# Performance work log

Hardware: AMD Instinct MI355X
Metric: run time of the kernel (lower is better)

Reference implementation:

```python
import math
from functools import partial

import jax
import jax.numpy as jnp
import numpy as np

DS = 128            # domain_size (cells per side); original used 600
PD = 1.0            # particle diameter d == grid spacing
KN = 500000.0       # normal stiffness
MASS = 1.0
DT = 1e-4
FS = 5              # filter (stencil) size -> 5x5x5 shifts
_ALPHA = -math.log(0.7) / math.pi
_GAMMA = _ALPHA / math.sqrt(_ALPHA ** 2 + 1.0)
ETA = 2.0 * _GAMMA * math.sqrt(KN * MASS)   # damping_coefficient_Eta
EPS = 1e-4          # torch.clamp(dist, 0.0001)
SHAPE = (1, 1, DS, DS, DS)


def setup_inputs() -> dict:
    rng = np.random.default_rng(0)
    occ = np.zeros((DS, DS, DS), np.float32)
    occ[1:-1, 1:-1, 1:-1] = (rng.random((DS - 2,) * 3) < 0.2).astype(np.float32)
    iz, iy, ix = np.meshgrid(np.arange(DS), np.arange(DS), np.arange(DS), indexing="ij")
    jit = lambda: (rng.random((DS,) * 3).astype(np.float32) - 0.5) * 0.4
    # occupied cells store their own coordinate (+jitter) so round(x/d) == cell index
    x = (occ * (ix.astype(np.float32) + jit())).astype(np.float32)
    y = (occ * (iy.astype(np.float32) + jit())).astype(np.float32)
    z = (occ * (iz.astype(np.float32) + jit())).astype(np.float32)
    vel = lambda: (occ * rng.normal(0.0, 0.5, (DS,) * 3)).astype(np.float32)
    asg = lambda a: jnp.asarray(a.reshape(SHAPE))
    return {
        "x_grid": asg(x), "y_grid": asg(y), "z_grid": asg(z),
        "vx_grid": asg(vel()), "vy_grid": asg(vel()), "vz_grid": asg(vel()),
        "mask": asg(occ),
    }


def _contrib(xg, yg, zg, vxg, vyg, vzg, shift):
    """Force contribution from one (i,j,k) stencil shift (torch.roll based)."""
    roll = lambda g: jnp.roll(g, shift, axis=(2, 3, 4))
    dx, dy, dz = xg - roll(xg), yg - roll(yg), zg - roll(zg)
    sq = dx * dx + dy * dy + dz * dz
    dist = jnp.sqrt(sq + 1e-20)  # tiny eps keeps sqrt grad finite at sq==0; value unchanged in fp32
    cd = jnp.maximum(dist, EPS)  # torch.clamp(dist, 0.0001)
    vn = ((vxg - roll(vxg)) * dx + (vyg - roll(vyg)) * dy + (vzg - roll(vzg)) * dz) / cd
    ov = dist < 2.0 * PD
    fx = jnp.where(ov, KN * (dist - 2.0 * PD) * dx / cd + ETA * vn * dx / cd, 0.0)
    fy = jnp.where(ov, KN * (dist - 2.0 * PD) * dy / cd + ETA * vn * dy / cd, 0.0)
    fz = jnp.where(ov, KN * (dist - 2.0 * PD) * dz / cd + ETA * vn * dz / cd, 0.0)
    return fx, fy, fz


def _forward(xg, yg, zg, vxg, vyg, vzg, mask):
    f32 = jnp.float32
    fx = jnp.zeros(SHAPE, f32)
    fy = jnp.zeros(SHAPE, f32)
    fz = jnp.zeros(SHAPE, f32)
    for i in range(FS):
        for j in range(FS):
            for k in range(FS):
                c = jax.checkpoint(partial(_contrib, shift=(k - 2, j - 2, i - 2)))
                dfx, dfy, dfz = c(xg, yg, zg, vxg, vyg, vzg)
                fx, fy, fz = fx + dfx, fy + dfy, fz + dfz
    # boundary overlap forces
    bl = ((xg != 0.0) & (xg < PD)).astype(f32)
    br = (xg > DS - 2.0 * PD).astype(f32)
    bb = ((yg != 0.0) & (yg < PD)).astype(f32)
    bt = (yg > DS - 2.0 * PD).astype(f32)
    bf = ((zg != 0.0) & (zg < PD)).astype(f32)
    bk = (zg > DS - 2.0 * PD).astype(f32)
    fxb = KN * bl * mask * (PD - xg) - KN * br * mask * (xg - DS + 2.0 * PD) - ETA * vxg * bl * mask - ETA * vxg * br * mask
    fyb = KN * bb * mask * (PD - yg) - KN * bt * mask * (yg - DS + 2.0 * PD) - ETA * vyg * bb * mask - ETA * vyg * bt * mask
    fzb = KN * bf * mask * (PD - zg) - KN * bk * mask * (zg - DS + 2.0 * PD) - ETA * vzg * bf * mask - ETA * vzg * bk * mask
    vxn = vxg + DT / MASS * mask * (-0.0 * MASS - fx + fxb)
    vyn = vyg + DT / MASS * mask * (-9.8 * MASS - fy + fyb)
    vzn = vzg + DT / MASS * mask * (-0.0 * MASS - fz + fzb)
    cell = lambda g: jnp.round(g / PD).astype(jnp.int32)
    cx0, cy0, cz0 = cell(xg), cell(yg), cell(zg)
    xn, yn, zn = xg + DT * vxn, yg + DT * vyn, zg + DT * vzn
    cx1, cy1, cz1 = cell(xn), cell(yn), cell(zn)
    # cell-list relocation: flatten to linear indices; invalid (empty) cells -> dump slot D3
    D3 = DS ** 3
    def lin(cz, cy, cx):
        v = (cx != 0) & (cy != 0) & (cz != 0)   # torch filters cell_* != 0
        return jnp.where(v, (cz * DS + cy) * DS + cx, D3).reshape(-1)
    lo = lin(cz0, cy0, cx0)
    ln = lin(cz1, cy1, cx1)
    pad = lambda g: jnp.concatenate([g.reshape(-1), jnp.zeros((1,), g.dtype)])
    unpad = lambda f: f[:D3].reshape(SHAPE)
    def move(g):
        gf = pad(g)
        return unpad(gf.at[lo].set(0.0).at[ln].set(gf[lo]))
    mask_n = unpad(pad(mask).at[lo].set(0.0).at[ln].set(1.0))
    return (move(xn), move(yn), move(zn), move(vxn), move(vyn), move(vzn), mask_n)


def reference(x_grid, y_grid, z_grid, vx_grid, vy_grid, vz_grid, mask):
    return _forward(x_grid, y_grid, z_grid, vx_grid, vy_grid, vz_grid, mask)
```

## Files before the change

kernel.cpp:

```cpp
#include <hip/hip_runtime.h>

#define DSZ   128
#define DMSK  127
#define D3    (DSZ * DSZ * DSZ)

#define KN_F   500000.0f
#define ETA_F  159.535258f
#define DT_F   1e-4f

#define TBX   32
#define TBY   4
#define TBZ   4
#define HALO  2
#define RS    37
#define PS    296
#define SLOTS 2368
#define NT    512
#define NHALO (36 * 8 * 8)
#define RES_S 520

struct OffTabs { int a[36]; int b[48]; int e[44]; };
constexpr OffTabs make_tabs() {
    OffTabs t{}; int na = 0, nb = 0, ne = 0;
    for (int dz = -2; dz <= 2; ++dz)
        for (int dy = -2; dy <= 2; ++dy)
            for (int dx = -2; dx <= 2; ++dx) {
                const int r2 = dz*dz + dy*dy + dx*dx;
                const int off = dz * PS + dy * RS + dx;
                if (r2 <= 4)      t.a[na++] = off;
                else if (r2 <= 6) t.b[nb++] = off;
                else              t.e[ne++] = off;
            }
    while (na < 36) t.a[na++] = 0;
    return t;
}
__constant__ OffTabs g_tabs = make_tabs();

__device__ __forceinline__ unsigned bf16_rne(float f) {
    unsigned u = __float_as_uint(f);
    u += 0x7fffu + ((u >> 16) & 1u);
    return u >> 16;
}
__device__ __forceinline__ unsigned packvv(float vy, float vz) {
    return bf16_rne(vy) | (bf16_rne(vz) << 16);
}
__device__ __forceinline__ float unpk_lo(unsigned w) { return __uint_as_float(w << 16); }
__device__ __forceinline__ float unpk_hi(unsigned w) { return __uint_as_float(w & 0xffff0000u); }

__device__ __forceinline__ void pair_full(
    const float4* __restrict__ lsp, const unsigned* __restrict__ lsv, int n,
    float px, float py, float pz, float vx, float vy, float vz,
    float& fx, float& fy, float& fz)
{
    const float4 q = lsp[n];
    const float ddx = px - q.x, ddy = py - q.y, ddz = pz - q.z;
    const float sq  = fmaf(ddx, ddx, fmaf(ddy, ddy, fmaf(ddz, ddz, 1e-20f)));
    const float rsd = __builtin_amdgcn_rsqf(sq);
    const float dist = sq * rsd;
    const unsigned w = lsv[n];
    const float vn = (fmaf(vx - q.w, ddx, fmaf(vy - unpk_lo(w), ddy, (vz - unpk_hi(w)) * ddz))) * rsd;
    float coef = fmaf(KN_F, dist - 2.0f, ETA_F * vn) * rsd;
    coef = (sq < 4.0f) ? coef : 0.0f;
    fx = fmaf(coef, ddx, fx);
    fy = fmaf(coef, ddy, fy);
    fz = fmaf(coef, ddz, fz);
}

__global__ __launch_bounds__(NT) void dem_tile(
    const float* __restrict__ X, const float* __restrict__ Y, const float* __restrict__ Z,
    const float* __restrict__ VX, const float* __restrict__ VY, const float* __restrict__ VZ,
    float* __restrict__ out)
{
    __shared__ float4 lsp[SLOTS];
    __shared__ unsigned lsv[SLOTS];
    __shared__ unsigned short plist[NT];
    __shared__ int loff[128];
    __shared__ unsigned int pcnt;
    __shared__ int nreloc;
    __shared__ int relocidx[8];
    __shared__ float relocval[8][7];

    const int tid = threadIdx.x;

    const unsigned raw = blockIdx.x;
    const unsigned xcd = raw & 7, loc = raw >> 3;
    const int bx = (int)((loc & 3) * TBX);
    const int by = (int)(((loc >> 2) & 31) * TBY);
    const int bz = (int)((xcd * 4 + (loc >> 7)) * TBZ);

    if (tid == 0) { pcnt = 0; nreloc = 0; }
    if (tid < 36) loff[tid] = g_tabs.a[tid];
    else if (tid < 84) loff[tid] = g_tabs.b[tid - 36];
    else if (tid < 128) loff[tid] = g_tabs.e[tid - 84];

    {
        const int bx2 = bx - HALO, by2 = by - HALO, bz2 = bz - HALO;
        #pragma unroll
        for (int it = 0; it < 5; ++it) {
            const int u = tid + it * NT;
            if (it < 4 || u < NHALO) {
                const int r  = (int)((unsigned)u / 36u);
                const int xl = u - r * 36;
                const int hz = r >> 3, hy = r & 7;
                const int gz = (bz2 + hz) & DMSK;
                const int gy = (by2 + hy) & DMSK;
                const int gx = (bx2 + xl) & DMSK;
                const int g  = (gz << 14) | (gy << 7) | gx;
                const int slot = hz * PS + hy * RS + xl;
                lsp[slot] = make_float4(X[g], Y[g], Z[g], VX[g]);
                lsv[slot] = packvv(VY[g], VZ[g]);
            }
        }
    }

    __syncthreads();

    const int tx = tid & 31, ty = (tid >> 5) & 3, tz = tid >> 7;
    const int lcc = (tz + HALO) * PS + (ty + HALO) * RS + (tx + HALO);
    const float4 qo = lsp[lcc];
    const bool occ = (qo.x != 0.0f);

    {
        const unsigned long long bmask = __ballot(occ);
        const int lane = tid & 63;
        const unsigned int prefix = (unsigned int)__popcll(bmask & ((1ull << lane) - 1ull));
        unsigned int base = 0;
        if (lane == 0) base = atomicAdd(&pcnt, (unsigned int)__popcll(bmask));
        base = __shfl(base, 0, 64);
        if (occ) plist[base + prefix] = (unsigned short)tid;
    }


    __syncthreads();

    const int n = (int)pcnt;
    const int grp = tid >> 2, sub = tid & 3;
    float fa[4], fb[4];
    int fcell[4] = { -1, -1, -1, -1 };

    int offA[9], offB[12];
    #pragma unroll
    for (int t = 0; t < 9; ++t)  offA[t] = loff[t * 4 + sub];
    #pragma unroll
    for (int t = 0; t < 12; ++t) offB[t] = loff[36 + t * 4 + sub];

    #pragma unroll
    for (int pp = 0; pp < 4; ++pp) {
        const int i = pp * 128 + grp;
        if (i >= n) break;
        const int p  = plist[i];
        const int px_ = p & 31, py_ = (p >> 5) & 3, pz_ = p >> 7;
        const int lc = (pz_ + HALO) * PS + (py_ + HALO) * RS + (px_ + HALO);
        const int cpg = ((bz + pz_) * DSZ + (by + py_)) * DSZ + (bx + px_);

        const float4 qc = lsp[lc];
        const unsigned wc = lsv[lc];
        const float px = qc.x, py = qc.y, pz = qc.z;
        const float vx = qc.w, vy = unpk_lo(wc), vz = unpk_hi(wc);
        float fx = 0.f, fy = 0.f, fz = 0.f;

        #pragma unroll
        for (int t = 0; t < 9; ++t)
            pair_full(lsp, lsv, lc + offA[t], px, py, pz, vx, vy, vz, fx, fy, fz);

        #pragma unroll
        for (int t = 0; t < 12; ++t) {
            const int nn = lc + offB[t];
            const float4 q = lsp[nn];
            const float ddx = px - q.x, ddy = py - q.y, ddz = pz - q.z;
            const float sq = fmaf(ddx, ddx, fmaf(ddy, ddy, fmaf(ddz, ddz, 1e-20f)));
            if (sq < 4.0f) {
                const float rsd = __builtin_amdgcn_rsqf(sq);
                const float dist = sq * rsd;
                const unsigned w = lsv[nn];
                const float vn = (fmaf(vx - q.w, ddx, fmaf(vy - unpk_lo(w), ddy, (vz - unpk_hi(w)) * ddz))) * rsd;
                const float coef = fmaf(KN_F, dist - 2.0f, ETA_F * vn) * rsd;
                fx = fmaf(coef, ddx, fx);
                fy = fmaf(coef, ddy, fy);
                fz = fmaf(coef, ddz, fz);
            }
        }

        const float sqo = px*px + py*py + pz*pz;
        if (sqo < 4.0f) {
            for (int t = sub; t < 44; t += 4)
                pair_full(lsp, lsv, lc + loff[84 + t], px, py, pz, vx, vy, vz, fx, fy, fz);
        }

        fx += __shfl_xor(fx, 1); fy += __shfl_xor(fy, 1); fz += __shfl_xor(fz, 1);
        fx += __shfl_xor(fx, 2); fy += __shfl_xor(fy, 2); fz += __shfl_xor(fz, 2);

        const float bl = (px != 0.0f && px < 1.0f)  ? 1.0f : 0.0f;
        const float br = (px > 126.0f)              ? 1.0f : 0.0f;
        const float bb = (py != 0.0f && py < 1.0f)  ? 1.0f : 0.0f;
        const float bt = (py > 126.0f)              ? 1.0f : 0.0f;
        const float bf = (pz != 0.0f && pz < 1.0f)  ? 1.0f : 0.0f;
        const float bk = (pz > 126.0f)              ? 1.0f : 0.0f;
        const float fxb = KN_F * bl * (1.0f - px) - KN_F * br * (px - 126.0f) - ETA_F * vx * (bl + br);
        const float fyb = KN_F * bb * (1.0f - py) - KN_F * bt * (py - 126.0f) - ETA_F * vy * (bb + bt);
        const float fzb = KN_F * bf * (1.0f - pz) - KN_F * bk * (pz - 126.0f) - ETA_F * vz * (bf + bk);

        const float vxn = vx + DT_F * (-fx + fxb);
        const float vyn = vy + DT_F * (-9.8f - fy + fyb);
        const float vzn = vz + DT_F * (-fz + fzb);
        const float xn = px + DT_F * vxn;
        const float yn = py + DT_F * vyn;
        const float zn = pz + DT_F * vzn;

        const int cx0 = (int)rintf(px), cy0 = (int)rintf(py), cz0 = (int)rintf(pz);
        const int cx1 = (int)rintf(xn), cy1 = (int)rintf(yn), cz1 = (int)rintf(zn);
        const int lo = (cx0 && cy0 && cz0) ? ((cz0 * DSZ + cy0) * DSZ + cx0) : D3;
        const int ln = (cx1 && cy1 && cz1) ? ((cz1 * DSZ + cy1) * DSZ + cx1) : D3;

        const bool zeroed = (lo == cpg) && (ln != cpg);
        const float mk = (ln == cpg) ? 1.0f : (zeroed ? 0.0f : 1.0f);
        const float o0 = zeroed ? 0.f : xn,  o1 = zeroed ? 0.f : yn,  o2 = zeroed ? 0.f : zn;
        const float o3 = zeroed ? 0.f : vxn, o4 = zeroed ? 0.f : vyn, o5 = zeroed ? 0.f : vzn;

        fcell[pp] = p;
        fa[pp] = (sub == 0) ? o0 : (sub == 1) ? o1 : (sub == 2) ? o2 : o3;
        fb[pp] = (sub == 0) ? o4 : (sub == 1) ? o5 : mk;

        if (sub == 0) {
            if (lo != cpg && lo < D3) {
                int s = atomicAdd(&nreloc, 1);
                if (s < 8) { relocidx[s] = lo; for (int f = 0; f < 7; ++f) relocval[s][f] = 0.f; }
            }
            if (ln != cpg && ln < D3) {
                int s = atomicAdd(&nreloc, 1);
                if (s < 8) {
                    relocidx[s] = ln;
                    relocval[s][0] = xn;  relocval[s][1] = yn;  relocval[s][2] = zn;
                    relocval[s][3] = vxn; relocval[s][4] = vyn; relocval[s][5] = vzn;
                    relocval[s][6] = 1.f;
                }
            }
        }
    }

    __syncthreads();

    float* res = (float*)lsp;
    if (!occ) {
        #pragma unroll
        for (int f = 0; f < 7; ++f) res[f * RES_S + tid] = 0.0f;
    }
    #pragma unroll
    for (int pp = 0; pp < 4; ++pp) {
        if (fcell[pp] >= 0) {
            res[sub * RES_S + fcell[pp]] = fa[pp];
            if (sub < 3) res[(sub + 4) * RES_S + fcell[pp]] = fb[pp];
        }
    }

    __syncthreads();

    for (int u = tid; u < 896; u += NT) {
        const int f = u >> 7, j = u & 127;
        const int cell = 4 * j;
        const int wtx = cell & 31, wty = (cell >> 5) & 3, wtz = cell >> 7;
        const float4 v = *(const float4*)(res + f * RES_S + cell);
        *(float4*)(out + f * D3 + ((bz + wtz) * DSZ + (by + wty)) * DSZ + bx + wtx) = v;
    }

    __syncthreads();
    const int nr = nreloc < 8 ? nreloc : 8;
    if (tid < nr) {
        const int idx = relocidx[tid];
        #pragma unroll
        for (int f = 0; f < 7; ++f) out[idx + f * D3] = relocval[tid][f];
    }
}

extern "C" void kernel_launch(void* const* d_in, const int* in_sizes, int n_in,
                              void* d_out, int out_size, void* d_ws, size_t ws_size,
                              hipStream_t stream)
{
    const float* X  = (const float*)d_in[0];
    const float* Y  = (const float*)d_in[1];
    const float* Z  = (const float*)d_in[2];
    const float* VX = (const float*)d_in[3];
    const float* VY = (const float*)d_in[4];
    const float* VZ = (const float*)d_in[5];
    float* out = (float*)d_out;

    dem_tile<<<(D3 / (TBX * TBY * TBZ)), NT, 0, stream>>>(X, Y, Z, VX, VY, VZ, out);
}
```

Before: 157.5 us.

## Permute stencil offsets to avoid LDS bank conflicts and batch neighbor loads

Reorders the per-lane stencil offset tables at compile time so that the four sub-lanes sharing a particle hit distinct residues mod 8, aiming to reduce LDS bank conflicts on the float4 neighbor loads. It also restructures the inner loops to issue several LDS loads back to back before doing the pair arithmetic, to expose more memory-level parallelism. It raises launch bounds to request 6 waves per SIMD, which may constrain register allocation and cause spills given the larger batches of live float4 values.

```diff
diff --git a/kernel.cpp b/kernel.cpp
--- a/kernel.cpp
+++ b/kernel.cpp
@@ -20,18 +20,49 @@
 #define RES_S 520
 
 struct OffTabs { int a[36]; int b[48]; int e[44]; };
+
+constexpr int residue8(int off) { return ((off % 8) + 8) % 8; }
+
+constexpr void permute_groups(const int* src, int n, int* dst) {
+    bool used[64] = {};
+    for (int g = 0; g < n / 4; ++g) {
+        int resmask = 0;
+        for (int s = 0; s < 4; ++s) {
+            int pick = -1, bestcnt = -1;
+            for (int i = 0; i < n; ++i) {
+                if (used[i]) continue;
+                const int r = residue8(src[i]);
+                if (resmask & (1 << r)) continue;
+                int cnt = 0;
+                for (int j = 0; j < n; ++j)
+                    if (!used[j] && residue8(src[j]) == r) ++cnt;
+                if (cnt > bestcnt) { bestcnt = cnt; pick = i; }
+            }
+            if (pick < 0)
+                for (int i = 0; i < n && pick < 0; ++i) if (!used[i]) pick = i;
+            used[pick] = true;
+            resmask |= (1 << residue8(src[pick]));
+            dst[g * 4 + s] = src[pick];
+        }
+    }
+}
+
 constexpr OffTabs make_tabs() {
-    OffTabs t{}; int na = 0, nb = 0, ne = 0;
+    OffTabs t{};
+    int ta[36] = {}; int tb[48] = {};
+    int na = 0, nb = 0, ne = 0;
     for (int dz = -2; dz <= 2; ++dz)
         for (int dy = -2; dy <= 2; ++dy)
             for (int dx = -2; dx <= 2; ++dx) {
                 const int r2 = dz*dz + dy*dy + dx*dx;
                 const int off = dz * PS + dy * RS + dx;
-                if (r2 <= 4)      t.a[na++] = off;
-                else if (r2 <= 6) t.b[nb++] = off;
+                if (r2 <= 4)      ta[na++] = off;
+                else if (r2 <= 6) tb[nb++] = off;
                 else              t.e[ne++] = off;
             }
-    while (na < 36) t.a[na++] = 0;
+    while (na < 36) ta[na++] = 0;
+    permute_groups(ta, 36, t.a);
+    permute_groups(tb, 48, t.b);
     return t;
 }
 __constant__ OffTabs g_tabs = make_tabs();
@@ -47,17 +78,15 @@
 __device__ __forceinline__ float unpk_lo(unsigned w) { return __uint_as_float(w << 16); }
 __device__ __forceinline__ float unpk_hi(unsigned w) { return __uint_as_float(w & 0xffff0000u); }
 
-__device__ __forceinline__ void pair_full(
-    const float4* __restrict__ lsp, const unsigned* __restrict__ lsv, int n,
+__device__ __forceinline__ void pair_qw(
+    const float4 q, const unsigned w,
     float px, float py, float pz, float vx, float vy, float vz,
     float& fx, float& fy, float& fz)
 {
-    const float4 q = lsp[n];
     const float ddx = px - q.x, ddy = py - q.y, ddz = pz - q.z;
     const float sq  = fmaf(ddx, ddx, fmaf(ddy, ddy, fmaf(ddz, ddz, 1e-20f)));
     const float rsd = __builtin_amdgcn_rsqf(sq);
     const float dist = sq * rsd;
-    const unsigned w = lsv[n];
     const float vn = (fmaf(vx - q.w, ddx, fmaf(vy - unpk_lo(w), ddy, (vz - unpk_hi(w)) * ddz))) * rsd;
     float coef = fmaf(KN_F, dist - 2.0f, ETA_F * vn) * rsd;
     coef = (sq < 4.0f) ? coef : 0.0f;
@@ -66,7 +95,15 @@
     fz = fmaf(coef, ddz, fz);
 }
 
-__global__ __launch_bounds__(NT) void dem_tile(
+__device__ __forceinline__ void pair_full(
+    const float4* __restrict__ lsp, const unsigned* __restrict__ lsv, int n,
+    float px, float py, float pz, float vx, float vy, float vz,
+    float& fx, float& fy, float& fz)
+{
+    pair_qw(lsp[n], lsv[n], px, py, pz, vx, vy, vz, fx, fy, fz);
+}
+
+__global__ __launch_bounds__(NT, 6) void dem_tile(
     const float* __restrict__ X, const float* __restrict__ Y, const float* __restrict__ Z,
     const float* __restrict__ VX, const float* __restrict__ VY, const float* __restrict__ VZ,
     float* __restrict__ out)
@@ -160,24 +197,39 @@
         float fx = 0.f, fy = 0.f, fz = 0.f;
 
         #pragma unroll
-        for (int t = 0; t < 9; ++t)
-            pair_full(lsp, lsv, lc + offA[t], px, py, pz, vx, vy, vz, fx, fy, fz);
-
-        #pragma unroll
-        for (int t = 0; t < 12; ++t) {
-            const int nn = lc + offB[t];
-            const float4 q = lsp[nn];
-            const float ddx = px - q.x, ddy = py - q.y, ddz = pz - q.z;
-            const float sq = fmaf(ddx, ddx, fmaf(ddy, ddy, fmaf(ddz, ddz, 1e-20f)));
-            if (sq < 4.0f) {
-                const float rsd = __builtin_amdgcn_rsqf(sq);
-                const float dist = sq * rsd;
-                const unsigned w = lsv[nn];
-                const float vn = (fmaf(vx - q.w, ddx, fmaf(vy - unpk_lo(w), ddy, (vz - unpk_hi(w)) * ddz))) * rsd;
-                const float coef = fmaf(KN_F, dist - 2.0f, ETA_F * vn) * rsd;
-                fx = fmaf(coef, ddx, fx);
-                fy = fmaf(coef, ddy, fy);
-                fz = fmaf(coef, ddz, fz);
+        for (int c = 0; c < 3; ++c) {
+            const int n0 = lc + offA[c * 3 + 0];
+            const int n1 = lc + offA[c * 3 + 1];
+            const int n2 = lc + offA[c * 3 + 2];
+            const float4  q0 = lsp[n0], q1 = lsp[n1], q2 = lsp[n2];
+            const unsigned w0 = lsv[n0], w1 = lsv[n1], w2 = lsv[n2];
+            pair_qw(q0, w0, px, py, pz, vx, vy, vz, fx, fy, fz);
+            pair_qw(q1, w1, px, py, pz, vx, vy, vz, fx, fy, fz);
+            pair_qw(q2, w2, px, py, pz, vx, vy, vz, fx, fy, fz);
+        }
+
+        #pragma unroll
+        for (int c = 0; c < 2; ++c) {
+            int nn[6]; float4 qb[6];
+            #pragma unroll
+            for (int t = 0; t < 6; ++t) {
+                nn[t] = lc + offB[c * 6 + t];
+                qb[t] = lsp[nn[t]];
+            }
+            #pragma unroll
+            for (int t = 0; t < 6; ++t) {
+                const float ddx = px - qb[t].x, ddy = py - qb[t].y, ddz = pz - qb[t].z;
+                const float sq = fmaf(ddx, ddx, fmaf(ddy, ddy, fmaf(ddz, ddz, 1e-20f)));
+                if (sq < 4.0f) {
+                    const float rsd = __builtin_amdgcn_rsqf(sq);
+                    const float dist = sq * rsd;
+                    const unsigned w = lsv[nn[t]];
+                    const float vn = (fmaf(vx - qb[t].w, ddx, fmaf(vy - unpk_lo(w), ddy, (vz - unpk_hi(w)) * ddz))) * rsd;
+                    const float coef = fmaf(KN_F, dist - 2.0f, ETA_F * vn) * rsd;
+                    fx = fmaf(coef, ddx, fx);
+                    fy = fmaf(coef, ddy, fy);
+                    fz = fmaf(coef, ddz, fz);
+                }
             }
         }
 
```

New measurement: 148.4 us, median of 3. 1.06x faster.
